# Optimization experiments

Measured on AMD Instinct MI355X. Metric: run time of the kernel, lower is better.

Reference implementation:

```python
import jax, jax.numpy as jnp
import numpy as np

B, F, CH, HW = 4, 16, 1280, 14
NPATCH = HW * HW            # 196
DIM, HEADS, DH = 1024, 16, 64
INNER = HEADS * DH          # 1024
DEPTH, NCLS = 2, 1
SEQ = 1 + F * NPATCH        # 3137
SCALE = DH ** -0.5


def layernorm(t, g, b):
    m = t.mean(-1, keepdims=True)
    v = ((t - m) ** 2).mean(-1, keepdims=True)
    return (t - m) / jnp.sqrt(v + 1e-5) * g + b


def masked_softmax(sim, mask):
    if mask is not None:
        sim = jnp.where(mask, sim, -jnp.finfo(sim.dtype).max)
    return jax.nn.softmax(sim, axis=-1)


def attention(xn, qkv_w, out_w, out_b, mode, frame_mask, cls_mask):
    # xn: [b, N, dim] (pre-normed). mode: 'time' or 'space'.
    b, N, _ = xn.shape
    qkv = xn @ qkv_w                         # [b, N, 3*inner]
    q, k, v = jnp.split(qkv, 3, axis=-1)
    sh = lambda t: t.reshape(b, N, HEADS, DH).transpose(0, 2, 1, 3).reshape(b * HEADS, N, DH)
    q, k, v = sh(q) * SCALE, sh(k), sh(v)
    # cls token attends to everything
    cls_sim = jnp.einsum('bid,bjd->bij', q[:, :1], k)          # [bh, 1, N]
    cls_out = jnp.einsum('bij,bjd->bid', masked_softmax(cls_sim, cls_mask), v)
    if mode == 'time':
        # (bh) (f n) d -> (bh n) f d
        tb = lambda t: t[:, 1:].reshape(-1, F, NPATCH, DH).transpose(0, 2, 1, 3).reshape(-1, F, DH)
        r, m = NPATCH, frame_mask
    else:
        # (bh) (f n) d -> (bh f) n d
        tb = lambda t: t[:, 1:].reshape(-1, NPATCH, DH)
        r, m = F, None
    q_, k_, v_ = tb(q), tb(k), tb(v)
    ck = jnp.repeat(k[:, :1], r, axis=0)     # broadcast cls k/v as prefix
    cv = jnp.repeat(v[:, :1], r, axis=0)
    k_ = jnp.concatenate([ck, k_], axis=1)
    v_ = jnp.concatenate([cv, v_], axis=1)
    sim = jnp.einsum('bid,bjd->bij', q_, k_)
    out = jnp.einsum('bij,bjd->bid', masked_softmax(sim, m), v_)
    if mode == 'time':
        out = out.reshape(b * HEADS, NPATCH, F, DH).transpose(0, 2, 1, 3).reshape(b * HEADS, F * NPATCH, DH)
    else:
        out = out.reshape(b * HEADS, F * NPATCH, DH)
    out = jnp.concatenate([cls_out, out], axis=1)              # [bh, N, d]
    out = out.reshape(b, HEADS, N, DH).transpose(0, 2, 1, 3).reshape(b, N, INNER)
    return out @ out_w + out_b


def _forward(x, patch_w, patch_b, cls_token, pos_emb,
             t_ng, t_nb, t_qkv, t_ow, t_ob,
             s_ng, s_nb, s_qkv, s_ow, s_ob,
             f_ng, f_nb, f_w1, f_b1, f_w2, f_b2,
             o_ng, o_nb, o_w, o_b, mask, identities_mask):
    b, f, c, h, w = x.shape
    n = h * w
    tokens = x.transpose(0, 1, 3, 4, 2).reshape(b, f * n, c) @ patch_w + patch_b
    xt = jnp.concatenate([jnp.broadcast_to(cls_token[None], (b, 1, DIM)), tokens], axis=1)
    N = xt.shape[1]
    xt = xt + pos_emb[:N]
    # frame mask: [b, f, f+1] -> [(b h n), f, f+1]
    fm = jnp.logical_and(mask[:, None, :], identities_mask)
    fm = jnp.pad(fm, ((0, 0), (0, 0), (1, 0)), constant_values=True)
    frame_mask = jnp.broadcast_to(fm[:, None, None], (b, HEADS, n, f, f + 1)).reshape(b * HEADS * n, f, f + 1)
    # cls mask: [(b h), 1, 1 + f*n]
    cm = jnp.broadcast_to(mask[:, None, :, None], (b, HEADS, f, n)).reshape(b * HEADS, 1, f * n)
    cm = jnp.pad(cm, ((0, 0), (0, 0), (1, 0)), constant_values=True)
    for i in range(DEPTH):
        y = attention(layernorm(xt, t_ng[i], t_nb[i]), t_qkv[i], t_ow[i], t_ob[i], 'time', frame_mask, cm)
        xt = xt + y
        y = attention(layernorm(xt, s_ng[i], s_nb[i]), s_qkv[i], s_ow[i], s_ob[i], 'space', None, cm)
        xt = xt + y
        hh = layernorm(xt, f_ng[i], f_nb[i]) @ f_w1[i] + f_b1[i]
        a, g = jnp.split(hh, 2, axis=-1)
        xt = xt + (a * jax.nn.gelu(g, approximate=False)) @ f_w2[i] + f_b2[i]
    cls = layernorm(xt[:, 0], o_ng, o_nb)
    return cls @ o_w + o_b


def setup_inputs() -> dict:
    key = jax.random.key(0)
    ks = jax.random.split(key, 16)
    rn = lambda k, shp: jax.random.normal(k, shp, dtype=jnp.float32) * 0.02
    return {
        'x': jax.random.normal(ks[0], (B, F, CH, HW, HW), dtype=jnp.float32),
        'mask': jnp.ones((B, F), dtype=bool),
        'identities_mask': jnp.ones((B, F, F), dtype=bool),
        'patch_w': rn(ks[1], (CH, DIM)), 'patch_b': jnp.zeros((DIM,), jnp.float32),
        'cls_token': rn(ks[2], (1, DIM)),
        'pos_emb': rn(ks[3], (SEQ, DIM)),
        't_ng': jnp.ones((DEPTH, DIM), jnp.float32), 't_nb': jnp.zeros((DEPTH, DIM), jnp.float32),
        't_qkv': rn(ks[4], (DEPTH, DIM, 3 * INNER)),
        't_ow': rn(ks[5], (DEPTH, INNER, DIM)), 't_ob': jnp.zeros((DEPTH, DIM), jnp.float32),
        's_ng': jnp.ones((DEPTH, DIM), jnp.float32), 's_nb': jnp.zeros((DEPTH, DIM), jnp.float32),
        's_qkv': rn(ks[6], (DEPTH, DIM, 3 * INNER)),
        's_ow': rn(ks[7], (DEPTH, INNER, DIM)), 's_ob': jnp.zeros((DEPTH, DIM), jnp.float32),
        'f_ng': jnp.ones((DEPTH, DIM), jnp.float32), 'f_nb': jnp.zeros((DEPTH, DIM), jnp.float32),
        'f_w1': rn(ks[8], (DEPTH, DIM, DIM * 8)), 'f_b1': jnp.zeros((DEPTH, DIM * 8), jnp.float32),
        'f_w2': rn(ks[9], (DEPTH, DIM * 4, DIM)), 'f_b2': jnp.zeros((DEPTH, DIM), jnp.float32),
        'o_ng': jnp.ones((DIM,), jnp.float32), 'o_nb': jnp.zeros((DIM,), jnp.float32),
        'o_w': rn(ks[10], (DIM, NCLS)), 'o_b': jnp.zeros((NCLS,), jnp.float32),
    }


def reference(x, mask, identities_mask, patch_w, patch_b, cls_token, pos_emb,
              t_ng, t_nb, t_qkv, t_ow, t_ob,
              s_ng, s_nb, s_qkv, s_ow, s_ob,
              f_ng, f_nb, f_w1, f_b1, f_w2, f_b2,
              o_ng, o_nb, o_w, o_b):
    return _forward(x, patch_w, patch_b, cls_token, pos_emb,
                    t_ng, t_nb, t_qkv, t_ow, t_ob,
                    s_ng, s_nb, s_qkv, s_ow, s_ob,
                    f_ng, f_nb, f_w1, f_b1, f_w2, f_b2,
                    o_ng, o_nb, o_w, o_b, mask, identities_mask)
```

## Files before the change

### kernel.cpp

```cpp
#include <hip/hip_runtime.h>


typedef unsigned short u16;
typedef __bf16 bf16x8 __attribute__((ext_vector_type(8)));
typedef float f32x4 __attribute__((ext_vector_type(4)));
typedef u16 u16x8 __attribute__((ext_vector_type(8)));

#define SEQ   3137
#define ROWS  12548
#define MPAD  12672
#define NTOK  12544
#define NCC   16
#define CHK   197

__device__ __forceinline__ u16 f2b(float f) {
  union { float f; unsigned u; } v; v.f = f;
  unsigned r = v.u + 0x7FFFu + ((v.u >> 16) & 1u);
  return (u16)(r >> 16);
}
__device__ __forceinline__ float b2f(u16 u) {
  union { unsigned u; float f; } v; v.u = ((unsigned)u) << 16;
  return v.f;
}
__device__ __forceinline__ float gelu_f(float g) {
  return 0.5f * g * (1.0f + erff(g * 0.70710678118654752f));
}
__device__ __forceinline__ bool read_bool(const void* p, int idx) {
  const unsigned* w = (const unsigned*)p;
  unsigned w0 = w[0];
  if (w0 == 1u || w0 == 0u) return ((const int*)p)[idx] != 0;
  if (w0 == 0x3F800000u) return w[idx] != 0;
  return ((const unsigned char*)p)[idx] != 0;
}

typedef const __attribute__((address_space(1))) void GVOID;
typedef __attribute__((address_space(3))) void LVOID;
__device__ __forceinline__ void gload_lds16(const void* g, void* l) {
  __builtin_amdgcn_global_load_lds((GVOID*)g, (LVOID*)l, 16, 0, 0);
}

template<int MODE>
__global__ __launch_bounds__(256) void gemm_bt(
    const u16* __restrict__ A, const u16* __restrict__ Bt,
    const float* __restrict__ bias,
    float* __restrict__ Cf, u16* __restrict__ Cb,
    int Mact, int N, int K)
{
  __shared__ char smem[65536];
  const int tid  = threadIdx.x;
  const int lane = tid & 63, wid = tid >> 6;
  const int wm = wid >> 1, wn = wid & 1;
  const long arow0 = (long)blockIdx.y * 128;
  const long brow0 = (long)blockIdx.x * 128;

  const int  s_row = tid >> 3;
  const int  s_swz = ((tid & 7) << 4) ^ (((tid >> 5) & 1) << 5);
  const char* Ag = (const char*)A + (arow0 + s_row) * (long)K * 2 + s_swz;
  const char* Bg = (const char*)Bt + (brow0 + s_row) * (long)K * 2 + s_swz;

  f32x4 acc[4][4] = {};
  const int rd_row_a = wm * 64 + (lane & 15);
  const int rd_row_b = wn * 64 + (lane & 15);
  const int rd_kb    = (lane >> 4) << 4;
  const int swzr     = ((lane >> 2) & 1) << 5;

  const int NT = K >> 6;
#pragma unroll
  for (int i = 0; i < 4; ++i) {
    gload_lds16(Ag + (long)i * 32 * K * 2, smem + wid * 1024 + i * 4096);
    gload_lds16(Bg + (long)i * 32 * K * 2, smem + 16384 + wid * 1024 + i * 4096);
  }
  __syncthreads();

  for (int t = 0; t < NT; ++t) {
    const int cur = t & 1;
    if (t + 1 < NT) {
      const long kb = (long)(t + 1) * 128;
      char* dst = smem + (cur ^ 1) * 32768 + wid * 1024;
#pragma unroll
      for (int i = 0; i < 4; ++i) {
        gload_lds16(Ag + kb + (long)i * 32 * K * 2, dst + i * 4096);
        gload_lds16(Bg + kb + (long)i * 32 * K * 2, dst + 16384 + i * 4096);
      }
    }
    const char* Ab = smem + cur * 32768;
    const char* Bb = Ab + 16384;
#pragma unroll
    for (int ks = 0; ks < 2; ++ks) {
      bf16x8 af[4], bfr[4];
#pragma unroll
      for (int mi = 0; mi < 4; ++mi)
        af[mi] = *(const bf16x8*)(Ab + (rd_row_a + mi * 16) * 128 + ((ks * 64 + rd_kb) ^ swzr));
#pragma unroll
      for (int ni = 0; ni < 4; ++ni)
        bfr[ni] = *(const bf16x8*)(Bb + (rd_row_b + ni * 16) * 128 + ((ks * 64 + rd_kb) ^ swzr));
#pragma unroll
      for (int mi = 0; mi < 4; ++mi)
#pragma unroll
        for (int ni = 0; ni < 4; ++ni)
          acc[mi][ni] = __builtin_amdgcn_mfma_f32_16x16x32_bf16(af[mi], bfr[ni], acc[mi][ni], 0, 0, 0);
    }
    __syncthreads();
  }

  const int ccol0 = (int)brow0 + wn * 64 + (lane & 15);
  const int rsub  = (lane >> 4) * 4;
  float bv[4];
#pragma unroll
  for (int ni = 0; ni < 4; ++ni) bv[ni] = bias ? bias[ccol0 + ni * 16] : 0.0f;
#pragma unroll
  for (int mi = 0; mi < 4; ++mi) {
#pragma unroll
    for (int r = 0; r < 4; ++r) {
      long row = arow0 + wm * 64 + mi * 16 + rsub + r;
      if (row < Mact) {
#pragma unroll
        for (int ni = 0; ni < 4; ++ni) {
          float v = acc[mi][ni][r] + bv[ni];
          long idx = row * (long)N + ccol0 + ni * 16;
          if (MODE == 0)      Cf[idx] = v;
          else if (MODE == 1) Cf[idx] += v;
          else                Cb[idx] = f2b(v);
        }
      }
    }
  }
}

__global__ __launch_bounds__(256) void gemm_w1_fused(
    const u16* __restrict__ A, const u16* __restrict__ Bt,
    const float* __restrict__ bias, u16* __restrict__ HACT, int Mact)
{
  __shared__ char smem[65536];
  const int K = 1024;
  const int tid  = threadIdx.x;
  const int lane = tid & 63, wid = tid >> 6;
  const int wm = wid >> 1, wn = wid & 1;
  const long arow0 = (long)blockIdx.y * 128;
  const long brow0 = (long)blockIdx.x * 128;

  const int  s_row = tid >> 3;
  const int  s_swz = ((tid & 7) << 4) ^ (((tid >> 5) & 1) << 5);
  const char* Ag = (const char*)A + (arow0 + s_row) * (long)K * 2 + s_swz;
  const char* Bg = (const char*)Bt + (brow0 + s_row) * (long)K * 2 + s_swz;

  f32x4 acc[4][4] = {};
  const int rd_row_a = wm * 64 + (lane & 15);
  const int rd_row_b = wn * 64 + (lane & 15);
  const int rd_kb    = (lane >> 4) << 4;
  const int swzr     = ((lane >> 2) & 1) << 5;

  const int NT = K >> 6;
#pragma unroll
  for (int i = 0; i < 4; ++i) {
    gload_lds16(Ag + (long)i * 32 * K * 2, smem + wid * 1024 + i * 4096);
    gload_lds16(Bg + (long)i * 32 * K * 2, smem + 16384 + wid * 1024 + i * 4096);
  }
  __syncthreads();

  for (int t = 0; t < NT; ++t) {
    const int cur = t & 1;
    if (t + 1 < NT) {
      const long kb = (long)(t + 1) * 128;
      char* dst = smem + (cur ^ 1) * 32768 + wid * 1024;
#pragma unroll
      for (int i = 0; i < 4; ++i) {
        gload_lds16(Ag + kb + (long)i * 32 * K * 2, dst + i * 4096);
        gload_lds16(Bg + kb + (long)i * 32 * K * 2, dst + 16384 + i * 4096);
      }
    }
    const char* Ab = smem + cur * 32768;
    const char* Bb = Ab + 16384;
#pragma unroll
    for (int ks = 0; ks < 2; ++ks) {
      bf16x8 af[4], bfr[4];
#pragma unroll
      for (int mi = 0; mi < 4; ++mi)
        af[mi] = *(const bf16x8*)(Ab + (rd_row_a + mi * 16) * 128 + ((ks * 64 + rd_kb) ^ swzr));
#pragma unroll
      for (int ni = 0; ni < 4; ++ni)
        bfr[ni] = *(const bf16x8*)(Bb + (rd_row_b + ni * 16) * 128 + ((ks * 64 + rd_kb) ^ swzr));
#pragma unroll
      for (int mi = 0; mi < 4; ++mi)
#pragma unroll
        for (int ni = 0; ni < 4; ++ni)
          acc[mi][ni] = __builtin_amdgcn_mfma_f32_16x16x32_bf16(af[mi], bfr[ni], acc[mi][ni], 0, 0, 0);
    }
    __syncthreads();
  }

  float* gx = (float*)smem;
  const int colb  = lane & 15;
  const int rsub  = (lane >> 4) * 4;
  const int cbase = blockIdx.x * 64;
  float bv[4];
#pragma unroll
  for (int ni = 0; ni < 4; ++ni)
    bv[ni] = bias[(wn ? 4096 : 0) + cbase + ni * 16 + colb];

  if (wn == 1) {
#pragma unroll
    for (int mi = 0; mi < 4; ++mi)
#pragma unroll
      for (int r = 0; r < 4; ++r) {
        int rl = mi * 16 + rsub + r;
#pragma unroll
        for (int ni = 0; ni < 4; ++ni)
          gx[(wm * 64 + rl) * 68 + ni * 16 + colb] = acc[mi][ni][r] + bv[ni];
      }
  }
  __syncthreads();
  if (wn == 0) {
#pragma unroll
    for (int mi = 0; mi < 4; ++mi)
#pragma unroll
      for (int r = 0; r < 4; ++r) {
        int rl = mi * 16 + rsub + r;
        long row = arow0 + wm * 64 + rl;
        if (row < Mact) {
#pragma unroll
          for (int ni = 0; ni < 4; ++ni) {
            float a = acc[mi][ni][r] + bv[ni];
            float g = gx[(wm * 64 + rl) * 68 + ni * 16 + colb];
            HACT[row * 4096L + cbase + ni * 16 + colb] = f2b(a * gelu_f(g));
          }
        }
      }
  }
}

__global__ __launch_bounds__(256) void transpose_cvt(
    const float* __restrict__ src, u16* __restrict__ dst,
    int R, int C, long sstride, long dstride)
{
  src += (long)blockIdx.z * sstride;
  dst += (long)blockIdx.z * dstride;
  __shared__ float tile[32][33];
  const int r0 = blockIdx.y * 32, c0 = blockIdx.x * 32;
  const int tx = threadIdx.x & 31, ty = threadIdx.x >> 5;
#pragma unroll
  for (int i = 0; i < 32; i += 8) {
    int r = r0 + ty + i, c = c0 + tx;
    if (r < R && c < C) tile[ty + i][tx] = src[(long)r * C + c];
  }
  __syncthreads();
#pragma unroll
  for (int i = 0; i < 32; i += 8) {
    int c = c0 + ty + i, r = r0 + tx;
    if (c < C && r < R) dst[(long)c * R + r] = f2b(tile[tx][ty + i]);
  }
}

__global__ __launch_bounds__(256) void transpose_w1(
    const float* __restrict__ src, u16* __restrict__ dst)
{
  __shared__ float tile[32][33];
  const int r0 = blockIdx.y * 32, c0 = blockIdx.x * 32;
  const int tx = threadIdx.x & 31, ty = threadIdx.x >> 5;
#pragma unroll
  for (int i = 0; i < 32; i += 8)
    tile[ty + i][tx] = src[(long)(r0 + ty + i) * 8192 + c0 + tx];
  __syncthreads();
#pragma unroll
  for (int i = 0; i < 32; i += 8) {
    int n = c0 + ty + i;
    int np = (n < 4096) ? ((n >> 6) * 128 + (n & 63))
                        : (((n - 4096) >> 6) * 128 + 64 + ((n - 4096) & 63));
    dst[(long)np * 1024 + r0 + tx] = f2b(tile[tx][ty + i]);
  }
}

__global__ __launch_bounds__(256) void build_xt(
    const float* __restrict__ TOK, const float* __restrict__ cls,
    const float* __restrict__ pos, float* __restrict__ XT)
{
  const int row = blockIdx.x, tid = threadIdx.x;
  const int b = row / SEQ, s = row % SEQ;
  float4 p = ((const float4*)(pos + (long)s * 1024))[tid];
  float4 t;
  if (s == 0) t = ((const float4*)cls)[tid];
  else        t = ((const float4*)(TOK + ((long)b * 3136 + (s - 1)) * 1024))[tid];
  float4 r; r.x = t.x + p.x; r.y = t.y + p.y; r.z = t.z + p.z; r.w = t.w + p.w;
  ((float4*)(XT + (long)row * 1024))[tid] = r;
}

__global__ __launch_bounds__(256) void ln_rows(
    const float* __restrict__ X, const float* __restrict__ g,
    const float* __restrict__ b, u16* __restrict__ Y)
{
  const int row = blockIdx.x, tid = threadIdx.x;
  const int lane = tid & 63, wid = tid >> 6;
  float4 x = ((const float4*)(X + (long)row * 1024))[tid];
  float s = x.x + x.y + x.z + x.w;
  float q = x.x * x.x + x.y * x.y + x.z * x.z + x.w * x.w;
#pragma unroll
  for (int o = 32; o; o >>= 1) { s += __shfl_xor(s, o); q += __shfl_xor(q, o); }
  __shared__ float ls[4], lq[4];
  if (lane == 0) { ls[wid] = s; lq[wid] = q; }
  __syncthreads();
  s = ls[0] + ls[1] + ls[2] + ls[3];
  q = lq[0] + lq[1] + lq[2] + lq[3];
  const float mean = s * (1.0f / 1024.0f);
  const float rstd = rsqrtf(q * (1.0f / 1024.0f) - mean * mean + 1e-5f);
  float4 gg = ((const float4*)g)[tid];
  float4 bb = ((const float4*)b)[tid];
  ushort4 o4;
  o4.x = f2b((x.x - mean) * rstd * gg.x + bb.x);
  o4.y = f2b((x.y - mean) * rstd * gg.y + bb.y);
  o4.z = f2b((x.z - mean) * rstd * gg.z + bb.z);
  o4.w = f2b((x.w - mean) * rstd * gg.w + bb.w);
  ((ushort4*)(Y + (long)row * 1024))[tid] = o4;
}

__global__ __launch_bounds__(256) void attn_cls_part(
    const u16* __restrict__ QKV, float* __restrict__ PART, const void* __restrict__ maskp)
{
  const int c = blockIdx.x, bh = blockIdx.y;
  const int b = bh >> 4, h = bh & 15;
  const long rowbase = (long)b * SEQ;
  const int tid = threadIdx.x, lane = tid & 63, w = tid >> 6;
  const int rs = lane >> 3, c8 = lane & 7;
  const int start = c * CHK;
  const int end = (start + CHK < SEQ) ? start + CHK : SEQ;

  float qf[8];
  {
    u16x8 qv = *(const u16x8*)(QKV + rowbase * 3072 + h * 64 + c8 * 8);
#pragma unroll
    for (int i = 0; i < 8; ++i) qf[i] = b2f(qv[i]) * 0.125f;
  }

  float m_run = -3.4e38f, s_run = 0.f;
  float acc[8] = {};

  for (int j8 = start + w * 8; j8 < end; j8 += 32) {
    int j = j8 + rs;
    bool valid = (j < end);
    int jc = valid ? j : (end - 1);
    const u16* kp = QKV + (rowbase + jc) * 3072 + 1024 + h * 64 + c8 * 8;
    u16x8 kv = *(const u16x8*)kp;
    u16x8 vv = *(const u16x8*)(kp + 1024);
    float sim = 0.f;
#pragma unroll
    for (int i = 0; i < 8; ++i) sim += b2f(kv[i]) * qf[i];
    sim += __shfl_xor(sim, 1); sim += __shfl_xor(sim, 2); sim += __shfl_xor(sim, 4);
    bool ok = valid && ((jc == 0) || read_bool(maskp, b * 16 + (jc - 1) / 196));
    float simv = ok ? sim : -3.4e38f;
    float mx = simv;
    mx = fmaxf(mx, __shfl_xor(mx, 8));
    mx = fmaxf(mx, __shfl_xor(mx, 16));
    mx = fmaxf(mx, __shfl_xor(mx, 32));
    float new_m = fmaxf(m_run, mx);
    float scale = __expf(m_run - new_m);
    float p = ok ? __expf(simv - new_m) : 0.f;
    m_run = new_m;
    s_run = s_run * scale + p;
#pragma unroll
    for (int i = 0; i < 8; ++i) acc[i] = acc[i] * scale + p * b2f(vv[i]);
  }
#pragma unroll
  for (int o = 8; o <= 32; o <<= 1) {
    s_run += __shfl_xor(s_run, o);
#pragma unroll
    for (int i = 0; i < 8; ++i) acc[i] += __shfl_xor(acc[i], o);
  }

  __shared__ float sm_m[4], sm_s[4], sm_a[4][64];
  if (lane == 0) { sm_m[w] = m_run; sm_s[w] = s_run; }
  if (rs == 0) {
#pragma unroll
    for (int i = 0; i < 8; ++i) sm_a[w][c8 * 8 + i] = acc[i];
  }
  __syncthreads();
  if (tid < 64) {
    float M = fmaxf(fmaxf(sm_m[0], sm_m[1]), fmaxf(sm_m[2], sm_m[3]));
    float S = 0.f, A = 0.f;
#pragma unroll
    for (int ww = 0; ww < 4; ++ww) {
      float e = __expf(sm_m[ww] - M);
      S += sm_s[ww] * e;
      A += sm_a[ww][tid] * e;
    }
    float* outp = PART + ((long)bh * NCC + c) * 72;
    outp[tid] = A;
    if (tid == 0) { outp[64] = M; outp[65] = S; }
  }
}

__global__ __launch_bounds__(64) void attn_cls_comb(
    const float* __restrict__ PART, u16* __restrict__ ATT)
{
  const int bh = blockIdx.x, b = bh >> 4, h = bh & 15;
  const int d = threadIdx.x;
  float M = -3.4e38f;
#pragma unroll
  for (int c = 0; c < NCC; ++c) M = fmaxf(M, PART[((long)bh * NCC + c) * 72 + 64]);
  float S = 0.f, A = 0.f;
#pragma unroll
  for (int c = 0; c < NCC; ++c) {
    const float* p = PART + ((long)bh * NCC + c) * 72;
    float e = __expf(p[64] - M);
    S += p[65] * e;
    A += p[d] * e;
  }
  ATT[((long)b * SEQ) * 1024 + h * 64 + d] = f2b(A / S);
}

__global__ __launch_bounds__(256) void attn_time(
    const u16* __restrict__ QKV, u16* __restrict__ ATT,
    const void* __restrict__ maskp, const void* __restrict__ idmp)
{
  const int g = blockIdx.x;
  const int n = g % 196;
  const int bh = g / 196;
  const int h = bh & 15, b = bh >> 4;
  const long rowbase = (long)b * SEQ;
  const int tid = threadIdx.x;
  __shared__ float q_s[16][65], k_s[17][65], v_s[17][65], p_s[16][18];
  for (int idx = tid; idx < 16 * 64; idx += 256) {
    int i = idx >> 6, d = idx & 63;
    q_s[i][d] = b2f(QKV[(rowbase + 1 + i * 196 + n) * 3072 + h * 64 + d]) * 0.125f;
  }
  for (int idx = tid; idx < 17 * 64; idx += 256) {
    int j = idx >> 6, d = idx & 63;
    long kr = (j == 0) ? rowbase : (rowbase + 1 + (long)(j - 1) * 196 + n);
    k_s[j][d] = b2f(QKV[kr * 3072 + 1024 + h * 64 + d]);
    v_s[j][d] = b2f(QKV[kr * 3072 + 2048 + h * 64 + d]);
  }
  __syncthreads();
#pragma unroll
  for (int pp = 0; pp < 2; ++pp) {
    int idx = tid + pp * 256;
    if (idx < 272) {
      int i = idx / 17, j = idx % 17;
      float s = 0.f;
      for (int d = 0; d < 64; ++d) s += q_s[i][d] * k_s[j][d];
      bool ok = (j == 0) ||
                (read_bool(maskp, b * 16 + (j - 1)) && read_bool(idmp, (b * 16 + i) * 16 + (j - 1)));
      p_s[i][j] = ok ? s : -3.4e38f;
    }
  }
  __syncthreads();
  if (tid < 16) {
    float m = -3.4e38f;
    for (int j = 0; j < 17; ++j) m = fmaxf(m, p_s[tid][j]);
    float su = 0.f;
    for (int j = 0; j < 17; ++j) { float e = __expf(p_s[tid][j] - m); p_s[tid][j] = e; su += e; }
    float inv = 1.0f / su;
    for (int j = 0; j < 17; ++j) p_s[tid][j] *= inv;
  }
  __syncthreads();
  for (int idx = tid; idx < 1024; idx += 256) {
    int i = idx >> 6, d = idx & 63;
    float o = 0.f;
#pragma unroll
    for (int j = 0; j < 17; ++j) o += p_s[i][j] * v_s[j][d];
    ATT[(rowbase + 1 + i * 196 + n) * 1024 + h * 64 + d] = f2b(o);
  }
}

__global__ __launch_bounds__(256) void attn_space(
    const u16* __restrict__ QKV, u16* __restrict__ ATT)
{
  const int g = blockIdx.x;
  const int fr = g & 15, bh = g >> 4;
  const int h = bh & 15, b = bh >> 4;
  const long rowbase = (long)b * SEQ;
  const long qbase = rowbase + 1 + (long)fr * 196;
  const int tid = threadIdx.x, lane = tid & 63, wid = tid >> 6;

  __shared__ u16 Ks[208][72];
  __shared__ u16 Vt[64][232];
  __shared__ u16 Ps[4][16][232];

  for (int c = tid; c < 197 * 8; c += 256) {
    int row = c >> 3, k8 = c & 7;
    long kr = (row == 0) ? rowbase : (qbase + row - 1);
    *(u16x8*)&Ks[row][k8 * 8] = *(const u16x8*)(QKV + kr * 3072 + 1024 + h * 64 + k8 * 8);
  }
  for (int c = tid; c < 64 * 35; c += 256) {
    int d = c / 35, k = 197 + c % 35;
    Vt[d][k] = 0;
  }
  for (int c = tid; c < 4 * 16 * 24; c += 256) {
    int w = c / (16 * 24), rem = c % (16 * 24);
    Ps[w][rem / 24][208 + rem % 24] = 0;
  }
  for (int c = tid; c < 197 * 64; c += 256) {
    int k = c >> 6, d = c & 63;
    long vr = (k == 0) ? rowbase : (qbase + k - 1);
    Vt[d][k] = QKV[vr * 3072 + 2048 + h * 64 + d];
  }
  __syncthreads();

  const int cl = lane & 15, hi = lane >> 4;
  for (int mt = wid; mt < 13; mt += 4) {
    int qi0 = mt * 16 + cl;
    long qrow = qbase + (qi0 < 196 ? qi0 : 0);
    const u16* qp = QKV + qrow * 3072 + h * 64 + hi * 8;
    bf16x8 af0 = *(const bf16x8*)qp;
    bf16x8 af1 = *(const bf16x8*)(qp + 32);

    f32x4 acc[13];
#pragma unroll
    for (int nt = 0; nt < 13; ++nt) {
      acc[nt] = (f32x4){0.f, 0.f, 0.f, 0.f};
      bf16x8 b0 = *(const bf16x8*)&Ks[nt * 16 + cl][hi * 8];
      acc[nt] = __builtin_amdgcn_mfma_f32_16x16x32_bf16(af0, b0, acc[nt], 0, 0, 0);
      bf16x8 b1 = *(const bf16x8*)&Ks[nt * 16 + cl][32 + hi * 8];
      acc[nt] = __builtin_amdgcn_mfma_f32_16x16x32_bf16(af1, b1, acc[nt], 0, 0, 0);
    }
    float mx[4] = {-3.4e38f, -3.4e38f, -3.4e38f, -3.4e38f};
#pragma unroll
    for (int nt = 0; nt < 13; ++nt) {
      int col = nt * 16 + cl;
#pragma unroll
      for (int r = 0; r < 4; ++r) {
        float s = acc[nt][r] * 0.125f;
        if (col >= 197) s = -3.4e38f;
        acc[nt][r] = s;
        mx[r] = fmaxf(mx[r], s);
      }
    }
#pragma unroll
    for (int r = 0; r < 4; ++r) {
#pragma unroll
      for (int o = 8; o; o >>= 1) mx[r] = fmaxf(mx[r], __shfl_xor(mx[r], o));
    }
    float sum[4] = {0.f, 0.f, 0.f, 0.f};
#pragma unroll
    for (int nt = 0; nt < 13; ++nt) {
      int col = nt * 16 + cl;
#pragma unroll
      for (int r = 0; r < 4; ++r) {
        float p = __expf(acc[nt][r] - mx[r]);
        sum[r] += p;
        Ps[wid][hi * 4 + r][col] = f2b(p);
      }
    }
    float inv[4];
#pragma unroll
    for (int r = 0; r < 4; ++r) {
#pragma unroll
      for (int o = 8; o; o >>= 1) sum[r] += __shfl_xor(sum[r], o);
      inv[r] = 1.0f / sum[r];
    }
    f32x4 ov[4];
#pragma unroll
    for (int dt = 0; dt < 4; ++dt) ov[dt] = (f32x4){0.f, 0.f, 0.f, 0.f};
#pragma unroll
    for (int ks = 0; ks < 7; ++ks) {
      bf16x8 pa = *(const bf16x8*)&Ps[wid][cl][ks * 32 + hi * 8];
#pragma unroll
      for (int dt = 0; dt < 4; ++dt) {
        bf16x8 vb = *(const bf16x8*)&Vt[dt * 16 + cl][ks * 32 + hi * 8];
        ov[dt] = __builtin_amdgcn_mfma_f32_16x16x32_bf16(pa, vb, ov[dt], 0, 0, 0);
      }
    }
#pragma unroll
    for (int r = 0; r < 4; ++r) {
      int qi = mt * 16 + hi * 4 + r;
      if (qi < 196) {
        long orow = (qbase + qi) * 1024 + h * 64;
#pragma unroll
        for (int dt = 0; dt < 4; ++dt)
          ATT[orow + dt * 16 + cl] = f2b(ov[dt][r] * inv[r]);
      }
    }
  }
}

__global__ __launch_bounds__(256) void final_head(
    const float* __restrict__ XT, const float* __restrict__ g,
    const float* __restrict__ b, const float* __restrict__ ow,
    const float* __restrict__ ob, float* __restrict__ out)
{
  const int bb = blockIdx.x, tid = threadIdx.x;
  const int lane = tid & 63, wid = tid >> 6;
  float4 x = ((const float4*)(XT + (long)bb * SEQ * 1024))[tid];
  float s = x.x + x.y + x.z + x.w;
  float q = x.x * x.x + x.y * x.y + x.z * x.z + x.w * x.w;
#pragma unroll
  for (int o = 32; o; o >>= 1) { s += __shfl_xor(s, o); q += __shfl_xor(q, o); }
  __shared__ float ls[4], lq[4], lt[4];
  if (lane == 0) { ls[wid] = s; lq[wid] = q; }
  __syncthreads();
  s = ls[0] + ls[1] + ls[2] + ls[3];
  q = lq[0] + lq[1] + lq[2] + lq[3];
  const float mean = s * (1.0f / 1024.0f);
  const float rstd = rsqrtf(q * (1.0f / 1024.0f) - mean * mean + 1e-5f);
  float4 gg = ((const float4*)g)[tid];
  float4 bv = ((const float4*)b)[tid];
  float4 wv = ((const float4*)ow)[tid];
  float t = ((x.x - mean) * rstd * gg.x + bv.x) * wv.x
          + ((x.y - mean) * rstd * gg.y + bv.y) * wv.y
          + ((x.z - mean) * rstd * gg.z + bv.z) * wv.z
          + ((x.w - mean) * rstd * gg.w + bv.w) * wv.w;
#pragma unroll
  for (int o = 32; o; o >>= 1) t += __shfl_xor(t, o);
  if (lane == 0) lt[wid] = t;
  __syncthreads();
  if (tid == 0) out[bb] = lt[0] + lt[1] + lt[2] + lt[3] + ob[0];
}

extern "C" void kernel_launch(void* const* d_in, const int* in_sizes, int n_in,
                              void* d_out, int out_size, void* d_ws, size_t ws_size,
                              hipStream_t stream) {
  const float* x       = (const float*)d_in[0];
  const void*  maskp   = d_in[1];
  const void*  idmp    = d_in[2];
  const float* patch_w = (const float*)d_in[3];
  const float* patch_b = (const float*)d_in[4];
  const float* cls_tok = (const float*)d_in[5];
  const float* pos_emb = (const float*)d_in[6];
  const float* t_ng = (const float*)d_in[7];
  const float* t_nb = (const float*)d_in[8];
  const float* t_qkv = (const float*)d_in[9];
  const float* t_ow = (const float*)d_in[10];
  const float* t_ob = (const float*)d_in[11];
  const float* s_ng = (const float*)d_in[12];
  const float* s_nb = (const float*)d_in[13];
  const float* s_qkv = (const float*)d_in[14];
  const float* s_ow = (const float*)d_in[15];
  const float* s_ob = (const float*)d_in[16];
  const float* f_ng = (const float*)d_in[17];
  const float* f_nb = (const float*)d_in[18];
  const float* f_w1 = (const float*)d_in[19];
  const float* f_b1 = (const float*)d_in[20];
  const float* f_w2 = (const float*)d_in[21];
  const float* f_b2 = (const float*)d_in[22];
  const float* o_ng = (const float*)d_in[23];
  const float* o_nb = (const float*)d_in[24];
  const float* o_w  = (const float*)d_in[25];
  const float* o_b  = (const float*)d_in[26];
  float* out = (float*)d_out;

  const size_t szXT   = (size_t)ROWS * 1024 * 4;
  const size_t szXNA  = (size_t)MPAD * 1024 * 2;
  const size_t szBIG  = (size_t)MPAD * 4096 * 2;
  const size_t szWBUF = (size_t)8192 * 1024 * 2;
  size_t off = 0;
  auto take = [&](size_t b) { size_t o = off; off += (b + 255) & ~(size_t)255; return o; };
  char* base = (char*)d_ws;
  float* XT  = (float*)(base + take(szXT));
  u16*  XNA  = (u16*)(base + take(szXNA));
  char* BIG  = base + take(szBIG);
  u16*  WBUF = (u16*)(base + take(szWBUF));
  if (off > ws_size) return;

  u16*   QKV  = (u16*)BIG;
  u16*   HACT = (u16*)BIG;
  u16*   Xtr  = (u16*)BIG;
  float* TOK  = (float*)(BIG + (size_t)40 * 1024 * 1024);
  float* PART = (float*)(BIG + (size_t)MPAD * 3072 * 2);

  auto tr = [&](const float* s, u16* d, int R, int C) {
    dim3 gr((C + 31) / 32, (R + 31) / 32, 1);
    transpose_cvt<<<gr, 256, 0, stream>>>(s, d, R, C, 0, 0);
  };

  {
    dim3 gr((196 + 31) / 32, (1280 + 31) / 32, 64);
    transpose_cvt<<<gr, 256, 0, stream>>>(x, Xtr, 1280, 196, 1280L * 196, 196L * 1280);
  }
  tr(patch_w, WBUF, 1280, 1024);
  gemm_bt<0><<<dim3(8, 98), 256, 0, stream>>>(Xtr, WBUF, patch_b, TOK, nullptr, NTOK, 1024, 1280);
  build_xt<<<ROWS, 256, 0, stream>>>(TOK, cls_tok, pos_emb, XT);

  for (int L = 0; L < 2; ++L) {
    tr(t_qkv + (size_t)L * 1024 * 3072, WBUF, 1024, 3072);
    ln_rows<<<ROWS, 256, 0, stream>>>(XT, t_ng + L * 1024, t_nb + L * 1024, XNA);
    gemm_bt<2><<<dim3(24, 99), 256, 0, stream>>>(XNA, WBUF, nullptr, nullptr, QKV, MPAD, 3072, 1024);
    tr(t_ow + (size_t)L * 1024 * 1024, WBUF, 1024, 1024);
    attn_cls_part<<<dim3(NCC, 64), 256, 0, stream>>>(QKV, PART, maskp);
    attn_cls_comb<<<64, 64, 0, stream>>>(PART, XNA);
    attn_time<<<NTOK, 256, 0, stream>>>(QKV, XNA, maskp, idmp);
    gemm_bt<1><<<dim3(8, 99), 256, 0, stream>>>(XNA, WBUF, t_ob + L * 1024, XT, nullptr, ROWS, 1024, 1024);
    tr(s_qkv + (size_t)L * 1024 * 3072, WBUF, 1024, 3072);
    ln_rows<<<ROWS, 256, 0, stream>>>(XT, s_ng + L * 1024, s_nb + L * 1024, XNA);
    gemm_bt<2><<<dim3(24, 99), 256, 0, stream>>>(XNA, WBUF, nullptr, nullptr, QKV, MPAD, 3072, 1024);
    tr(s_ow + (size_t)L * 1024 * 1024, WBUF, 1024, 1024);
    attn_cls_part<<<dim3(NCC, 64), 256, 0, stream>>>(QKV, PART, maskp);
    attn_cls_comb<<<64, 64, 0, stream>>>(PART, XNA);
    attn_space<<<1024, 256, 0, stream>>>(QKV, XNA);
    gemm_bt<1><<<dim3(8, 99), 256, 0, stream>>>(XNA, WBUF, s_ob + L * 1024, XT, nullptr, ROWS, 1024, 1024);
    transpose_w1<<<dim3(256, 32), 256, 0, stream>>>(f_w1 + (size_t)L * 1024 * 8192, WBUF);
    ln_rows<<<ROWS, 256, 0, stream>>>(XT, f_ng + L * 1024, f_nb + L * 1024, XNA);
    gemm_w1_fused<<<dim3(64, 99), 256, 0, stream>>>(XNA, WBUF, f_b1 + L * 8192, HACT, ROWS);
    tr(f_w2 + (size_t)L * 4096 * 1024, WBUF, 4096, 1024);
    gemm_bt<1><<<dim3(8, 99), 256, 0, stream>>>(HACT, WBUF, f_b2 + L * 1024, XT, nullptr, ROWS, 1024, 4096);
  }
  final_head<<<4, 256, 0, stream>>>(XT, o_ng, o_nb, o_w, o_b, out);
}
```

Measured before the change: 2.152 ms.

## Use 256x256-tile 512-thread GEMM with deeper prefetch for QKV and FFN-in

Replaces the 128x128-tile GEMMs for the QKV projections and the fused GELU-gated FFN-in GEMM with a 256x256-tile kernel using 8 waves and 128 KB of LDS. Loads are double-buffered two tiles ahead, with explicit vmcnt waits and raw barriers. The larger tile raises arithmetic intensity and cuts global/LDS traffic per MFMA. The gated-GELU epilogue is restructured so odd column-waves stage the gate half in LDS. The normalized-activation buffer is padded to 12800 rows to cover the larger M tiles. In exchange, occupancy drops, fewer blocks fill the grid, and the large static LDS may limit residency to one block per CU.

```diff
diff --git a/kernel.cpp b/kernel.cpp
--- a/kernel.cpp
+++ b/kernel.cpp
@@ -9,6 +9,7 @@
 #define SEQ   3137
 #define ROWS  12548
 #define MPAD  12672
+#define MPADA 12800
 #define NTOK  12544
 #define NCC   16
 #define CHK   197
@@ -127,102 +128,121 @@
   }
 }
 
-__global__ __launch_bounds__(256) void gemm_w1_fused(
+#define G256_LOOP                                                                        \
+  const int K = 1024, NT = 16;                                                           \
+  const int tid = threadIdx.x;                                                           \
+  const int lane = tid & 63, wid = tid >> 6;                                             \
+  const int wr = wid >> 2, wc = wid & 3;                                                 \
+  const long arow0 = (long)blockIdx.y * 256;                                             \
+  const long brow0 = (long)blockIdx.x * 256;                                             \
+  const int s_row = tid >> 3;                                                            \
+  const int s_swz = ((tid & 7) << 4) ^ (((tid >> 5) & 1) << 5);                          \
+  const char* Ag = (const char*)A + (arow0 + s_row) * (long)K * 2 + s_swz;               \
+  const char* Bg = (const char*)Bt + (brow0 + s_row) * (long)K * 2 + s_swz;              \
+  auto issue = [&](int t, int buf) {                                                     \
+    const long kb = (long)t * 128;                                                       \
+    char* d = smem + buf * 65536 + tid * 16;                                             \
+    _Pragma("unroll")                                                                    \
+    for (int i = 0; i < 4; ++i) {                                                        \
+      gload_lds16(Ag + kb + (long)(i * 64) * K * 2, d + i * 8192);                       \
+      gload_lds16(Bg + kb + (long)(i * 64) * K * 2, d + 32768 + i * 8192);               \
+    }                                                                                    \
+  };                                                                                     \
+  f32x4 acc[8][4] = {};                                                                  \
+  const int fr = lane & 15;                                                              \
+  const int rd_kb = (lane >> 4) << 4;                                                    \
+  const int swzr = ((lane >> 2) & 1) << 5;                                               \
+  issue(0, 0); issue(1, 1);                                                              \
+  for (int t = 0; t < NT; ++t) {                                                         \
+    if (t + 1 < NT) asm volatile("s_waitcnt vmcnt(8)" ::: "memory");                     \
+    else            asm volatile("s_waitcnt vmcnt(0)" ::: "memory");                     \
+    __builtin_amdgcn_sched_barrier(0);                                                   \
+    __builtin_amdgcn_s_barrier();                                                        \
+    __builtin_amdgcn_sched_barrier(0);                                                   \
+    const char* Ab = smem + (t & 1) * 65536;                                             \
+    const char* Bb = Ab + 32768;                                                         \
+    _Pragma("unroll")                                                                    \
+    for (int ks = 0; ks < 2; ++ks) {                                                     \
+      bf16x8 af[8], bfr[4];                                                              \
+      _Pragma("unroll")                                                                  \
+      for (int mi = 0; mi < 8; ++mi)                                                     \
+        af[mi] = *(const bf16x8*)(Ab + (wr * 128 + mi * 16 + fr) * 128 +                 \
+                                  ((ks * 64 + rd_kb) ^ swzr));                           \
+      _Pragma("unroll")                                                                  \
+      for (int ni = 0; ni < 4; ++ni)                                                     \
+        bfr[ni] = *(const bf16x8*)(Bb + (wc * 64 + ni * 16 + fr) * 128 +                 \
+                                   ((ks * 64 + rd_kb) ^ swzr));                          \
+      _Pragma("unroll")                                                                  \
+      for (int mi = 0; mi < 8; ++mi)                                                     \
+        _Pragma("unroll")                                                                \
+        for (int ni = 0; ni < 4; ++ni)                                                   \
+          acc[mi][ni] = __builtin_amdgcn_mfma_f32_16x16x32_bf16(af[mi], bfr[ni],         \
+                                                                acc[mi][ni], 0, 0, 0);   \
+    }                                                                                    \
+    __builtin_amdgcn_sched_barrier(0);                                                   \
+    __builtin_amdgcn_s_barrier();                                                        \
+    __builtin_amdgcn_sched_barrier(0);                                                   \
+    if (t + 2 < NT) issue(t + 2, t & 1);                                                 \
+  }
+
+__global__ __launch_bounds__(512, 2) void gemm256_bt(
+    const u16* __restrict__ A, const u16* __restrict__ Bt,
+    u16* __restrict__ Cb, int Mact, int N)
+{
+  __shared__ char smem[131072];
+  G256_LOOP
+  const int cl = fr, hi = lane >> 4;
+#pragma unroll
+  for (int mi = 0; mi < 8; ++mi)
+#pragma unroll
+    for (int r = 0; r < 4; ++r) {
+      long row = arow0 + wr * 128 + mi * 16 + hi * 4 + r;
+      if (row < Mact) {
+#pragma unroll
+        for (int ni = 0; ni < 4; ++ni)
+          Cb[row * (long)N + brow0 + wc * 64 + ni * 16 + cl] = f2b(acc[mi][ni][r]);
+      }
+    }
+}
+
+__global__ __launch_bounds__(512, 2) void gemm256_w1(
     const u16* __restrict__ A, const u16* __restrict__ Bt,
     const float* __restrict__ bias, u16* __restrict__ HACT, int Mact)
 {
-  __shared__ char smem[65536];
-  const int K = 1024;
-  const int tid  = threadIdx.x;
-  const int lane = tid & 63, wid = tid >> 6;
-  const int wm = wid >> 1, wn = wid & 1;
-  const long arow0 = (long)blockIdx.y * 128;
-  const long brow0 = (long)blockIdx.x * 128;
-
-  const int  s_row = tid >> 3;
-  const int  s_swz = ((tid & 7) << 4) ^ (((tid >> 5) & 1) << 5);
-  const char* Ag = (const char*)A + (arow0 + s_row) * (long)K * 2 + s_swz;
-  const char* Bg = (const char*)Bt + (brow0 + s_row) * (long)K * 2 + s_swz;
-
-  f32x4 acc[4][4] = {};
-  const int rd_row_a = wm * 64 + (lane & 15);
-  const int rd_row_b = wn * 64 + (lane & 15);
-  const int rd_kb    = (lane >> 4) << 4;
-  const int swzr     = ((lane >> 2) & 1) << 5;
-
-  const int NT = K >> 6;
-#pragma unroll
-  for (int i = 0; i < 4; ++i) {
-    gload_lds16(Ag + (long)i * 32 * K * 2, smem + wid * 1024 + i * 4096);
-    gload_lds16(Bg + (long)i * 32 * K * 2, smem + 16384 + wid * 1024 + i * 4096);
-  }
-  __syncthreads();
-
-  for (int t = 0; t < NT; ++t) {
-    const int cur = t & 1;
-    if (t + 1 < NT) {
-      const long kb = (long)(t + 1) * 128;
-      char* dst = smem + (cur ^ 1) * 32768 + wid * 1024;
-#pragma unroll
-      for (int i = 0; i < 4; ++i) {
-        gload_lds16(Ag + kb + (long)i * 32 * K * 2, dst + i * 4096);
-        gload_lds16(Bg + kb + (long)i * 32 * K * 2, dst + 16384 + i * 4096);
-      }
-    }
-    const char* Ab = smem + cur * 32768;
-    const char* Bb = Ab + 16384;
-#pragma unroll
-    for (int ks = 0; ks < 2; ++ks) {
-      bf16x8 af[4], bfr[4];
-#pragma unroll
-      for (int mi = 0; mi < 4; ++mi)
-        af[mi] = *(const bf16x8*)(Ab + (rd_row_a + mi * 16) * 128 + ((ks * 64 + rd_kb) ^ swzr));
-#pragma unroll
-      for (int ni = 0; ni < 4; ++ni)
-        bfr[ni] = *(const bf16x8*)(Bb + (rd_row_b + ni * 16) * 128 + ((ks * 64 + rd_kb) ^ swzr));
-#pragma unroll
-      for (int mi = 0; mi < 4; ++mi)
+  __shared__ char smem[131072];
+  G256_LOOP
+  const int cl = fr, hi = lane >> 4;
+  const int p = wc >> 1;
+  const int cbase = blockIdx.x * 128 + p * 64;
+  float* gx = (float*)smem + (wr * 2 + p) * 8192;
+  if (wc & 1) {
+#pragma unroll
+    for (int mi = 0; mi < 8; ++mi)
+#pragma unroll
+      for (int r = 0; r < 4; ++r) {
+        int rowl = mi * 16 + hi * 4 + r;
 #pragma unroll
         for (int ni = 0; ni < 4; ++ni)
-          acc[mi][ni] = __builtin_amdgcn_mfma_f32_16x16x32_bf16(af[mi], bfr[ni], acc[mi][ni], 0, 0, 0);
-    }
-    __syncthreads();
-  }
-
-  float* gx = (float*)smem;
-  const int colb  = lane & 15;
-  const int rsub  = (lane >> 4) * 4;
-  const int cbase = blockIdx.x * 64;
-  float bv[4];
-#pragma unroll
-  for (int ni = 0; ni < 4; ++ni)
-    bv[ni] = bias[(wn ? 4096 : 0) + cbase + ni * 16 + colb];
-
-  if (wn == 1) {
-#pragma unroll
-    for (int mi = 0; mi < 4; ++mi)
+          gx[rowl * 64 + ni * 16 + cl] = acc[mi][ni][r] + bias[4096 + cbase + ni * 16 + cl];
+      }
+  }
+  __syncthreads();
+  if (!(wc & 1)) {
+    float bv[4];
+#pragma unroll
+    for (int ni = 0; ni < 4; ++ni) bv[ni] = bias[cbase + ni * 16 + cl];
+#pragma unroll
+    for (int mi = 0; mi < 8; ++mi)
 #pragma unroll
       for (int r = 0; r < 4; ++r) {
-        int rl = mi * 16 + rsub + r;
-#pragma unroll
-        for (int ni = 0; ni < 4; ++ni)
-          gx[(wm * 64 + rl) * 68 + ni * 16 + colb] = acc[mi][ni][r] + bv[ni];
-      }
-  }
-  __syncthreads();
-  if (wn == 0) {
-#pragma unroll
-    for (int mi = 0; mi < 4; ++mi)
-#pragma unroll
-      for (int r = 0; r < 4; ++r) {
-        int rl = mi * 16 + rsub + r;
-        long row = arow0 + wm * 64 + rl;
+        int rowl = mi * 16 + hi * 4 + r;
+        long row = arow0 + wr * 128 + rowl;
         if (row < Mact) {
 #pragma unroll
           for (int ni = 0; ni < 4; ++ni) {
             float a = acc[mi][ni][r] + bv[ni];
-            float g = gx[(wm * 64 + rl) * 68 + ni * 16 + colb];
-            HACT[row * 4096L + cbase + ni * 16 + colb] = f2b(a * gelu_f(g));
+            float g = gx[rowl * 64 + ni * 16 + cl];
+            HACT[row * 4096L + cbase + ni * 16 + cl] = f2b(a * gelu_f(g));
           }
         }
       }
@@ -636,7 +656,7 @@
   float* out = (float*)d_out;
 
   const size_t szXT   = (size_t)ROWS * 1024 * 4;
-  const size_t szXNA  = (size_t)MPAD * 1024 * 2;
+  const size_t szXNA  = (size_t)MPADA * 1024 * 2;
   const size_t szBIG  = (size_t)MPAD * 4096 * 2;
   const size_t szWBUF = (size_t)8192 * 1024 * 2;
   size_t off = 0;
@@ -670,7 +690,7 @@
   for (int L = 0; L < 2; ++L) {
     tr(t_qkv + (size_t)L * 1024 * 3072, WBUF, 1024, 3072);
     ln_rows<<<ROWS, 256, 0, stream>>>(XT, t_ng + L * 1024, t_nb + L * 1024, XNA);
-    gemm_bt<2><<<dim3(24, 99), 256, 0, stream>>>(XNA, WBUF, nullptr, nullptr, QKV, MPAD, 3072, 1024);
+    gemm256_bt<<<dim3(12, 50), 512, 0, stream>>>(XNA, WBUF, QKV, ROWS, 3072);
     tr(t_ow + (size_t)L * 1024 * 1024, WBUF, 1024, 1024);
     attn_cls_part<<<dim3(NCC, 64), 256, 0, stream>>>(QKV, PART, maskp);
     attn_cls_comb<<<64, 64, 0, stream>>>(PART, XNA);
@@ -678,7 +698,7 @@
     gemm_bt<1><<<dim3(8, 99), 256, 0, stream>>>(XNA, WBUF, t_ob + L * 1024, XT, nullptr, ROWS, 1024, 1024);
     tr(s_qkv + (size_t)L * 1024 * 3072, WBUF, 1024, 3072);
     ln_rows<<<ROWS, 256, 0, stream>>>(XT, s_ng + L * 1024, s_nb + L * 1024, XNA);
-    gemm_bt<2><<<dim3(24, 99), 256, 0, stream>>>(XNA, WBUF, nullptr, nullptr, QKV, MPAD, 3072, 1024);
+    gemm256_bt<<<dim3(12, 50), 512, 0, stream>>>(XNA, WBUF, QKV, ROWS, 3072);
     tr(s_ow + (size_t)L * 1024 * 1024, WBUF, 1024, 1024);
     attn_cls_part<<<dim3(NCC, 64), 256, 0, stream>>>(QKV, PART, maskp);
     attn_cls_comb<<<64, 64, 0, stream>>>(PART, XNA);
@@ -686,7 +706,7 @@
     gemm_bt<1><<<dim3(8, 99), 256, 0, stream>>>(XNA, WBUF, s_ob + L * 1024, XT, nullptr, ROWS, 1024, 1024);
     transpose_w1<<<dim3(256, 32), 256, 0, stream>>>(f_w1 + (size_t)L * 1024 * 8192, WBUF);
     ln_rows<<<ROWS, 256, 0, stream>>>(XT, f_ng + L * 1024, f_nb + L * 1024, XNA);
-    gemm_w1_fused<<<dim3(64, 99), 256, 0, stream>>>(XNA, WBUF, f_b1 + L * 8192, HACT, ROWS);
+    gemm256_w1<<<dim3(32, 50), 512, 0, stream>>>(XNA, WBUF, f_b1 + L * 8192, HACT, ROWS);
     tr(f_w2 + (size_t)L * 4096 * 1024, WBUF, 4096, 1024);
     gemm_bt<1><<<dim3(8, 99), 256, 0, stream>>>(HACT, WBUF, f_b2 + L * 1024, XT, nullptr, ROWS, 1024, 4096);
   }
```

Result: slower. 2.221 ms (+3.2%).
